# Kernel tuning notes

Measured on AMD Instinct MI355X. Metric: run time of the kernel, lower is better.

Reference implementation:

```python
import jax, jax.numpy as jnp
import numpy as np

HARD_NUM = 700      # hardcoded self.hard_num in HardOIMLoss
OIM_SCALAR = 30.0   # oim_scalar init arg
N, D, P, Q = 4096, 256, 5532, 5000


def _l2norm(x):
    return x / jnp.linalg.norm(x, axis=-1, keepdims=True)


def setup_inputs() -> dict:
    key = jax.random.key(0)
    k1, k2, k3, k4, k5 = jax.random.split(key, 5)
    # OIM features and lookup tables are L2-normalized rows
    inputs = _l2norm(jax.random.normal(k1, (N, D), dtype=jnp.float32))
    lut = _l2norm(jax.random.normal(k2, (P, D), dtype=jnp.float32))
    cq = _l2norm(jax.random.normal(k3, (Q, D), dtype=jnp.float32))
    reliability = jax.random.uniform(k4, (P + Q,), dtype=jnp.float32)
    labels = jax.random.randint(k5, (N,), 0, P, dtype=jnp.int32)
    return {"inputs": inputs, "labels": labels, "lut": lut, "cq": cq,
            "reliability": reliability}


def reference(inputs, labels, lut, cq, reliability):
    # projected[n, c] = <inputs_n, table_c> * reliability_c ;  table = [lut; cq]
    table = jnp.concatenate([lut, cq], axis=0)            # [P+Q, D]
    projected = (inputs @ table.T) * reliability[None, :]  # [N, P+Q]
    C = projected.shape[1]
    # value at sorted-descending index HARD_NUM == (HARD_NUM+1)-th largest
    boundary = jax.lax.top_k(projected, HARD_NUM + 1)[0][:, -1]  # [N]
    hard_mask = projected >= boundary[:, None]
    label_mask = jnp.arange(C, dtype=labels.dtype)[None, :] == labels[:, None]
    mask = hard_mask | label_mask
    logits = jnp.where(mask, projected * OIM_SCALAR, -jnp.inf)
    # cross entropy (mean over rows); label column is always unmasked
    logZ = jax.scipy.special.logsumexp(logits, axis=1)
    tgt = jnp.take_along_axis(logits, labels[:, None].astype(jnp.int32), axis=1)[:, 0]
    return jnp.mean(logZ - tgt)
```

## Files before the change

### kernel.cpp

```cpp
#include <hip/hip_runtime.h>
#include <math.h>

#define N_ROWS 4096
#define DIM    256
#define P_SZ   5532
#define Q_SZ   5000
#define C_COLS 10532
#define TPAD   10624
#define PSTR   10560
#define K_SEL  701
#define SCALAR 30.0f

typedef __attribute__((ext_vector_type(8))) short   short8;
typedef __attribute__((ext_vector_type(4))) float   float4_t;
typedef __attribute__((ext_vector_type(4))) unsigned short ushort4_t;
typedef __attribute__((ext_vector_type(8))) unsigned short ushort8_t;

__device__ __forceinline__ unsigned short f2bf(float f) {
    unsigned u = __float_as_uint(f);
    unsigned r = u + 0x7FFFu + ((u >> 16) & 1u);
    return (unsigned short)(r >> 16);
}
__device__ __forceinline__ float bf2f(unsigned short u) {
    return __uint_as_float((unsigned)u << 16);
}
__device__ __forceinline__ unsigned key16(unsigned short u) {
    return (u & 0x8000u) ? (unsigned)(~u & 0xFFFFu) : (unsigned)(u | 0x8000u);
}
__device__ __forceinline__ float key2f16(unsigned key) {
    unsigned short b = (key & 0x8000u) ? (unsigned short)(key & 0x7FFFu)
                                       : (unsigned short)(~key & 0xFFFFu);
    return bf2f(b);
}
__device__ __forceinline__ void gload16(const void* g, void* l) {
    __builtin_amdgcn_global_load_lds(
        (const __attribute__((address_space(1))) unsigned int*)g,
        (__attribute__((address_space(3))) unsigned int*)l, 16, 0, 0);
}

__device__ __forceinline__ unsigned suffix_above(unsigned s, int lane, int wid,
                                                 unsigned* wsum) {
    unsigned incl = s;
    #pragma unroll
    for (int off = 1; off < 64; off <<= 1) {
        unsigned v = __shfl_down(incl, off, 64);
        if (lane + off < 64) incl += v;
    }
    unsigned wtot = __shfl(incl, 0, 64);
    if (lane == 0) wsum[wid] = wtot;
    __syncthreads();
    unsigned tail = 0;
    for (int w = wid + 1; w < 4; ++w) tail += wsum[w];
    return tail + (incl - s);
}

#define NIN_G  (N_ROWS * DIM / 4)
#define NTAB_G (TPAD * DIM / 4)

__global__ __launch_bounds__(256) void convert_bf16(
    const float* __restrict__ inputs, const float* __restrict__ lut,
    const float* __restrict__ cq, unsigned short* __restrict__ in_bf,
    unsigned short* __restrict__ tab_bf)
{
    const int g = blockIdx.x * 256 + threadIdx.x;
    if (g >= NIN_G + NTAB_G) return;
    float4_t v;
    unsigned short* dst;
    if (g < NIN_G) {
        v = *(const float4_t*)&inputs[(size_t)g * 4];
        dst = in_bf + (size_t)g * 4;
    } else {
        const int t = g - NIN_G;
        const int row = t >> 6;
        const int c4  = (t & 63) * 4;
        if (row < P_SZ)        v = *(const float4_t*)&lut[(size_t)row * DIM + c4];
        else if (row < C_COLS) v = *(const float4_t*)&cq[(size_t)(row - P_SZ) * DIM + c4];
        else                   v = (float4_t){0.f, 0.f, 0.f, 0.f};
        dst = tab_bf + (size_t)t * 4;
    }
    ushort4_t h = { f2bf(v.x), f2bf(v.y), f2bf(v.z), f2bf(v.w) };
    *(ushort4_t*)dst = h;
}

#define NWG_X 83
#define NWG_Y 32
#define NWG   (NWG_X * NWG_Y)

__global__ __launch_bounds__(256) void gemm_proj(
    const unsigned short* __restrict__ in_bf,
    const unsigned short* __restrict__ tab_bf,
    const float* __restrict__ rel,
    unsigned short* __restrict__ proj)
{
    __shared__ __align__(16) unsigned short At[128 * 64];
    __shared__ __align__(16) unsigned short Bt[128 * 64];

    const int tid  = threadIdx.x;
    const int lane = tid & 63, wid = tid >> 6;
    const int wm = wid >> 1, wn = wid & 1;

    const int phys = blockIdx.x;
    const int wg   = (phys & 7) * (NWG / 8) + (phys >> 3);
    const int bx   = wg >> 5;
    const int by   = wg & 31;
    const int row0 = by * 128, col0 = bx * 128;

    float4_t acc[4][4];
    #pragma unroll
    for (int i = 0; i < 4; ++i)
        #pragma unroll
        for (int j = 0; j < 4; ++j)
            acc[i][j] = (float4_t){0.f, 0.f, 0.f, 0.f};

    for (int k0 = 0; k0 < DIM; k0 += 64) {
        #pragma unroll
        for (int it = 0; it < 4; ++it) {
            const int g  = it * 256 + tid;
            const int r  = g >> 3;
            const int kb = ((g & 7) * 16) ^ ((r & 7) << 4);
            gload16(in_bf  + (size_t)(row0 + r) * DIM + k0 + (kb >> 1),
                    (char*)At + g * 16);
            gload16(tab_bf + (size_t)(col0 + r) * DIM + k0 + (kb >> 1),
                    (char*)Bt + g * 16);
        }
        __syncthreads();

        #pragma unroll
        for (int kk = 0; kk < 2; ++kk) {
            const int krow = lane & 15;
            const int kb   = kk * 64 + ((lane >> 4) << 4);
            short8 af[4], bfr[4];
            #pragma unroll
            for (int i = 0; i < 4; ++i) {
                const int r = wm * 64 + i * 16 + krow;
                af[i] = *(const short8*)((const char*)At + (r * 128 + (kb ^ ((r & 7) << 4))));
            }
            #pragma unroll
            for (int j = 0; j < 4; ++j) {
                const int r = wn * 64 + j * 16 + krow;
                bfr[j] = *(const short8*)((const char*)Bt + (r * 128 + (kb ^ ((r & 7) << 4))));
            }
            #pragma unroll
            for (int i = 0; i < 4; ++i)
                #pragma unroll
                for (int j = 0; j < 4; ++j)
                    acc[i][j] = __builtin_amdgcn_mfma_f32_16x16x32_bf16(af[i], bfr[j], acc[i][j], 0, 0, 0);
        }
        __syncthreads();
    }

    const int lr = (lane >> 4) << 2;
    const int lc = lane & 15;
    #pragma unroll
    for (int j = 0; j < 4; ++j) {
        const int col = col0 + wn * 64 + j * 16 + lc;
        if (col >= PSTR) continue;
        const bool pad = (col >= C_COLS);
        const float rl = pad ? 0.f : rel[col];
        #pragma unroll
        for (int i = 0; i < 4; ++i) {
            const int row = row0 + wm * 64 + i * 16 + lr;
            #pragma unroll
            for (int rr = 0; rr < 4; ++rr)
                proj[(size_t)(row + rr) * PSTR + col] =
                    pad ? (unsigned short)0xFF80u
                        : f2bf(acc[i][j][rr] * rl);
        }
    }
}

__global__ __launch_bounds__(256) void row_loss_kernel(
    const unsigned short* __restrict__ proj, const int* __restrict__ labels,
    float* __restrict__ row_loss)
{
    __shared__ __align__(16) unsigned short vals[PSTR];
    __shared__ unsigned hist[2048];
    __shared__ unsigned wsum[4];
    __shared__ unsigned wred[4];
    __shared__ float fred[4];
    __shared__ unsigned sel_b, sel_k;

    const int tid = threadIdx.x, lane = tid & 63, wid = tid >> 6;
    const int row = blockIdx.x;
    const ushort8_t* prow = (const ushort8_t*)(proj + (size_t)row * PSTR);

    for (int i = tid; i < 2048; i += 256) hist[i] = 0;
    __syncthreads();

    unsigned mkey = 0;
    for (int g = tid; g < PSTR / 8; g += 256) {
        const ushort8_t v = prow[g];
        *(ushort8_t*)&vals[g * 8] = v;
        #pragma unroll
        for (int e = 0; e < 8; ++e) {
            const unsigned key = key16(v[e]);
            mkey = max(mkey, key);
            atomicAdd(&hist[key >> 5], 1u);
        }
    }
    #pragma unroll
    for (int off = 1; off < 64; off <<= 1) {
        const unsigned t = __shfl_down(mkey, off, 64);
        if (lane + off < 64) mkey = max(mkey, t);
    }
    if (lane == 0) wred[wid] = mkey;
    __syncthreads();
    mkey = max(max(wred[0], wred[1]), max(wred[2], wred[3]));
    const float m = key2f16(mkey);

    unsigned k = K_SEL;

    {
        unsigned s = 0;
        #pragma unroll
        for (int b = 0; b < 8; ++b) s += hist[tid * 8 + b];
        unsigned cum = suffix_above(s, lane, wid, wsum);
        #pragma unroll
        for (int b = 7; b >= 0; --b) {
            const unsigned c = hist[tid * 8 + b];
            if (cum < k && cum + c >= k) { sel_b = (unsigned)(tid * 8 + b); sel_k = k - cum; }
            cum += c;
        }
    }
    __syncthreads();
    const unsigned b1 = sel_b; k = sel_k;
    if (tid < 32) hist[tid] = 0;
    __syncthreads();

    for (int g = tid; g < PSTR / 8; g += 256) {
        const ushort8_t v = *(const ushort8_t*)&vals[g * 8];
        #pragma unroll
        for (int e = 0; e < 8; ++e) {
            const unsigned key = key16(v[e]);
            if ((key >> 5) == b1) atomicAdd(&hist[key & 31u], 1u);
        }
    }
    __syncthreads();
    if (wid == 0) {
        const unsigned c = (lane < 32) ? hist[lane] : 0u;
        unsigned incl = c;
        #pragma unroll
        for (int off = 1; off < 64; off <<= 1) {
            const unsigned t = __shfl_down(incl, off, 64);
            if (lane + off < 64) incl += t;
        }
        const unsigned above = incl - c;
        if (lane < 32 && above < k && above + c >= k) sel_b = (unsigned)lane;
    }
    __syncthreads();
    const unsigned bkey = (b1 << 5) | sel_b;

    const float c2 = SCALAR * 1.4426950408889634f;
    float s = 0.f;
    for (int g = tid; g < PSTR / 8; g += 256) {
        const ushort8_t v = *(const ushort8_t*)&vals[g * 8];
        #pragma unroll
        for (int e = 0; e < 8; ++e)
            if (key16(v[e]) >= bkey) s += exp2f(c2 * (bf2f(v[e]) - m));
    }
    #pragma unroll
    for (int off = 1; off < 64; off <<= 1) {
        const float t = __shfl_down(s, off, 64);
        if (lane + off < 64) s += t;
    }
    if (lane == 0) fred[wid] = s;
    __syncthreads();

    if (tid == 0) {
        float total = fred[0] + fred[1] + fred[2] + fred[3];
        const unsigned short ul = vals[labels[row]];
        const float pl = bf2f(ul);
        if (key16(ul) < bkey) total += exp2f(c2 * (pl - m));
        row_loss[row] = SCALAR * m + logf(total) - SCALAR * pl;
    }
}

__global__ __launch_bounds__(256) void final_reduce(
    const float* __restrict__ row_loss, float* __restrict__ out)
{
    __shared__ float fred[4];
    const int tid = threadIdx.x, lane = tid & 63, wid = tid >> 6;
    float s = 0.f;
    for (int i = tid; i < N_ROWS; i += 256) s += row_loss[i];
    #pragma unroll
    for (int off = 1; off < 64; off <<= 1) {
        const float t = __shfl_down(s, off, 64);
        if (lane + off < 64) s += t;
    }
    if (lane == 0) fred[wid] = s;
    __syncthreads();
    if (tid == 0) out[0] = (fred[0] + fred[1] + fred[2] + fred[3]) / (float)N_ROWS;
}

extern "C" void kernel_launch(void* const* d_in, const int* in_sizes, int n_in,
                              void* d_out, int out_size, void* d_ws, size_t ws_size,
                              hipStream_t stream) {
    const float* inputs = (const float*)d_in[0];
    const int*   labels = (const int*)d_in[1];
    const float* lut    = (const float*)d_in[2];
    const float* cq     = (const float*)d_in[3];
    const float* rel    = (const float*)d_in[4];
    float* out = (float*)d_out;

    unsigned short* in_bf  = (unsigned short*)d_ws;
    unsigned short* tab_bf = in_bf  + (size_t)N_ROWS * DIM;
    unsigned short* proj   = tab_bf + (size_t)TPAD * DIM;
    float* rl_buf = (float*)(proj + (size_t)N_ROWS * PSTR);

    convert_bf16<<<(NIN_G + NTAB_G) / 256, 256, 0, stream>>>(inputs, lut, cq, in_bf, tab_bf);
    gemm_proj<<<NWG, 256, 0, stream>>>(in_bf, tab_bf, rel, proj);
    row_loss_kernel<<<N_ROWS, 256, 0, stream>>>(proj, labels, rl_buf);
    final_reduce<<<1, 256, 0, stream>>>(rl_buf, out);
}
```

Measured before the change: 115.4 us.

## Fuse exp-sum into histogram pass with fixed max shift; stage GEMM output through LDS

The GEMM epilogue now writes its bf16 tile to LDS and stores it to global memory as coalesced 16-byte rows, with the projection stride padded to the table pad width. The row-loss kernel drops the max reduction and the LDS row copy. It accumulates per-bucket exp sums alongside the histogram counts, using a fixed shift of 1.0 (which relies on |projected| <= 1 for normalized inputs and reliability <= 1), so the separate final exp pass is removed. The cost is a float atomic plus an exp for every element in the first pass, and the second pass now rereads the row from global memory.

```diff
diff --git a/kernel.cpp b/kernel.cpp
--- a/kernel.cpp
+++ b/kernel.cpp
@@ -7,9 +7,11 @@
 #define Q_SZ   5000
 #define C_COLS 10532
 #define TPAD   10624
-#define PSTR   10560
+#define PSTR   10624
+#define NGR    (PSTR / 8)
 #define K_SEL  701
 #define SCALAR 30.0f
+#define C2     (SCALAR * 1.4426950408889634f)
 
 typedef __attribute__((ext_vector_type(8))) short   short8;
 typedef __attribute__((ext_vector_type(4))) float   float4_t;
@@ -27,31 +29,10 @@
 __device__ __forceinline__ unsigned key16(unsigned short u) {
     return (u & 0x8000u) ? (unsigned)(~u & 0xFFFFu) : (unsigned)(u | 0x8000u);
 }
-__device__ __forceinline__ float key2f16(unsigned key) {
-    unsigned short b = (key & 0x8000u) ? (unsigned short)(key & 0x7FFFu)
-                                       : (unsigned short)(~key & 0xFFFFu);
-    return bf2f(b);
-}
 __device__ __forceinline__ void gload16(const void* g, void* l) {
     __builtin_amdgcn_global_load_lds(
         (const __attribute__((address_space(1))) unsigned int*)g,
         (__attribute__((address_space(3))) unsigned int*)l, 16, 0, 0);
-}
-
-__device__ __forceinline__ unsigned suffix_above(unsigned s, int lane, int wid,
-                                                 unsigned* wsum) {
-    unsigned incl = s;
-    #pragma unroll
-    for (int off = 1; off < 64; off <<= 1) {
-        unsigned v = __shfl_down(incl, off, 64);
-        if (lane + off < 64) incl += v;
-    }
-    unsigned wtot = __shfl(incl, 0, 64);
-    if (lane == 0) wsum[wid] = wtot;
-    __syncthreads();
-    unsigned tail = 0;
-    for (int w = wid + 1; w < 4; ++w) tail += wsum[w];
-    return tail + (incl - s);
 }
 
 #define NIN_G  (N_ROWS * DIM / 4)
@@ -85,6 +66,7 @@
 #define NWG_X 83
 #define NWG_Y 32
 #define NWG   (NWG_X * NWG_Y)
+#define CSTR  132
 
 __global__ __launch_bounds__(256) void gemm_proj(
     const unsigned short* __restrict__ in_bf,
@@ -92,8 +74,9 @@
     const float* __restrict__ rel,
     unsigned short* __restrict__ proj)
 {
-    __shared__ __align__(16) unsigned short At[128 * 64];
-    __shared__ __align__(16) unsigned short Bt[128 * 64];
+    __shared__ __align__(16) unsigned short smem[128 * CSTR];
+    unsigned short* At = smem;
+    unsigned short* Bt = smem + 128 * 64;
 
     const int tid  = threadIdx.x;
     const int lane = tid & 63, wid = tid >> 6;
@@ -153,19 +136,27 @@
     const int lc = lane & 15;
     #pragma unroll
     for (int j = 0; j < 4; ++j) {
-        const int col = col0 + wn * 64 + j * 16 + lc;
-        if (col >= PSTR) continue;
+        const int cl  = wn * 64 + j * 16 + lc;
+        const int col = col0 + cl;
         const bool pad = (col >= C_COLS);
         const float rl = pad ? 0.f : rel[col];
         #pragma unroll
         for (int i = 0; i < 4; ++i) {
-            const int row = row0 + wm * 64 + i * 16 + lr;
+            const int rbase = wm * 64 + i * 16 + lr;
             #pragma unroll
             for (int rr = 0; rr < 4; ++rr)
-                proj[(size_t)(row + rr) * PSTR + col] =
-                    pad ? (unsigned short)0xFF80u
-                        : f2bf(acc[i][j][rr] * rl);
-        }
+                smem[(rbase + rr) * CSTR + cl] =
+                    pad ? (unsigned short)0xFF80u : f2bf(acc[i][j][rr] * rl);
+        }
+    }
+    __syncthreads();
+    #pragma unroll
+    for (int it = 0; it < 8; ++it) {
+        const int g = it * 256 + tid;
+        const int r = g >> 4;
+        const int c8 = (g & 15) * 8;
+        *(ushort8_t*)(proj + (size_t)(row0 + r) * PSTR + col0 + c8) =
+            *(const ushort8_t*)&smem[r * CSTR + c8];
     }
 }
 
@@ -173,105 +164,103 @@
     const unsigned short* __restrict__ proj, const int* __restrict__ labels,
     float* __restrict__ row_loss)
 {
-    __shared__ __align__(16) unsigned short vals[PSTR];
     __shared__ unsigned hist[2048];
+    __shared__ float    bexp[2048];
+    __shared__ unsigned h2[32];
+    __shared__ float    e2[32];
     __shared__ unsigned wsum[4];
-    __shared__ unsigned wred[4];
-    __shared__ float fred[4];
+    __shared__ float    fsum[4];
     __shared__ unsigned sel_b, sel_k;
+    __shared__ float    sel_major, sel_minor;
 
     const int tid = threadIdx.x, lane = tid & 63, wid = tid >> 6;
     const int row = blockIdx.x;
     const ushort8_t* prow = (const ushort8_t*)(proj + (size_t)row * PSTR);
 
-    for (int i = tid; i < 2048; i += 256) hist[i] = 0;
-    __syncthreads();
-
-    unsigned mkey = 0;
-    for (int g = tid; g < PSTR / 8; g += 256) {
+    #pragma unroll
+    for (int i = tid; i < 2048; i += 256) { hist[i] = 0; bexp[i] = 0.f; }
+    if (tid < 32) { h2[tid] = 0; e2[tid] = 0.f; }
+    __syncthreads();
+
+    for (int g = tid; g < NGR; g += 256) {
         const ushort8_t v = prow[g];
-        *(ushort8_t*)&vals[g * 8] = v;
         #pragma unroll
         for (int e = 0; e < 8; ++e) {
             const unsigned key = key16(v[e]);
-            mkey = max(mkey, key);
+            const float ex = exp2f(C2 * (bf2f(v[e]) - 1.0f));
             atomicAdd(&hist[key >> 5], 1u);
-        }
-    }
-    #pragma unroll
-    for (int off = 1; off < 64; off <<= 1) {
-        const unsigned t = __shfl_down(mkey, off, 64);
-        if (lane + off < 64) mkey = max(mkey, t);
-    }
-    if (lane == 0) wred[wid] = mkey;
-    __syncthreads();
-    mkey = max(max(wred[0], wred[1]), max(wred[2], wred[3]));
-    const float m = key2f16(mkey);
-
-    unsigned k = K_SEL;
+            atomicAdd(&bexp[key >> 5], ex);
+        }
+    }
+    __syncthreads();
 
     {
-        unsigned s = 0;
-        #pragma unroll
-        for (int b = 0; b < 8; ++b) s += hist[tid * 8 + b];
-        unsigned cum = suffix_above(s, lane, wid, wsum);
+        const int t8 = tid * 8;
+        unsigned s = 0; float f = 0.f;
+        #pragma unroll
+        for (int b = 0; b < 8; ++b) { s += hist[t8 + b]; f += bexp[t8 + b]; }
+        unsigned ic = s; float fc = f;
+        #pragma unroll
+        for (int off = 1; off < 64; off <<= 1) {
+            const unsigned tc = __shfl_down(ic, off, 64);
+            const float    tf = __shfl_down(fc, off, 64);
+            if (lane + off < 64) { ic += tc; fc += tf; }
+        }
+        if (lane == 0) { wsum[wid] = ic; fsum[wid] = fc; }
+        __syncthreads();
+        unsigned cum = ic - s; float fcum = fc - f;
+        for (int w = wid + 1; w < 4; ++w) { cum += wsum[w]; fcum += fsum[w]; }
         #pragma unroll
         for (int b = 7; b >= 0; --b) {
-            const unsigned c = hist[tid * 8 + b];
-            if (cum < k && cum + c >= k) { sel_b = (unsigned)(tid * 8 + b); sel_k = k - cum; }
-            cum += c;
-        }
-    }
-    __syncthreads();
-    const unsigned b1 = sel_b; k = sel_k;
-    if (tid < 32) hist[tid] = 0;
-    __syncthreads();
-
-    for (int g = tid; g < PSTR / 8; g += 256) {
-        const ushort8_t v = *(const ushort8_t*)&vals[g * 8];
+            const unsigned c = hist[t8 + b];
+            if (cum < K_SEL && cum + c >= K_SEL) {
+                sel_b = (unsigned)(t8 + b); sel_k = K_SEL - cum; sel_major = fcum;
+            }
+            cum += c; fcum += bexp[t8 + b];
+        }
+    }
+    __syncthreads();
+    const unsigned b1 = sel_b;
+    const unsigned k2 = sel_k;
+    __syncthreads();
+
+    for (int g = tid; g < NGR; g += 256) {
+        const ushort8_t v = prow[g];
         #pragma unroll
         for (int e = 0; e < 8; ++e) {
             const unsigned key = key16(v[e]);
-            if ((key >> 5) == b1) atomicAdd(&hist[key & 31u], 1u);
+            if ((key >> 5) == b1) {
+                atomicAdd(&h2[key & 31u], 1u);
+                atomicAdd(&e2[key & 31u], exp2f(C2 * (bf2f(v[e]) - 1.0f)));
+            }
         }
     }
     __syncthreads();
     if (wid == 0) {
-        const unsigned c = (lane < 32) ? hist[lane] : 0u;
-        unsigned incl = c;
+        const unsigned c = (lane < 32) ? h2[lane] : 0u;
+        const float    f = (lane < 32) ? e2[lane] : 0.f;
+        unsigned ic = c; float fc = f;
         #pragma unroll
         for (int off = 1; off < 64; off <<= 1) {
-            const unsigned t = __shfl_down(incl, off, 64);
-            if (lane + off < 64) incl += t;
-        }
-        const unsigned above = incl - c;
-        if (lane < 32 && above < k && above + c >= k) sel_b = (unsigned)lane;
-    }
-    __syncthreads();
-    const unsigned bkey = (b1 << 5) | sel_b;
-
-    const float c2 = SCALAR * 1.4426950408889634f;
-    float s = 0.f;
-    for (int g = tid; g < PSTR / 8; g += 256) {
-        const ushort8_t v = *(const ushort8_t*)&vals[g * 8];
-        #pragma unroll
-        for (int e = 0; e < 8; ++e)
-            if (key16(v[e]) >= bkey) s += exp2f(c2 * (bf2f(v[e]) - m));
-    }
-    #pragma unroll
-    for (int off = 1; off < 64; off <<= 1) {
-        const float t = __shfl_down(s, off, 64);
-        if (lane + off < 64) s += t;
-    }
-    if (lane == 0) fred[wid] = s;
+            const unsigned tc = __shfl_down(ic, off, 64);
+            const float    tf = __shfl_down(fc, off, 64);
+            if (lane + off < 64) { ic += tc; fc += tf; }
+        }
+        const unsigned above = ic - c;
+        if (lane < 32 && above < k2 && above + c >= k2) {
+            sel_b = (unsigned)lane; sel_minor = fc;
+        }
+    }
     __syncthreads();
 
     if (tid == 0) {
-        float total = fred[0] + fred[1] + fred[2] + fred[3];
-        const unsigned short ul = vals[labels[row]];
+        const unsigned bkey = (b1 << 5) | sel_b;
+        float total = sel_major + sel_minor;
+        const unsigned short ul = *(const unsigned short*)
+            ((const unsigned short*)prow + labels[row]);
         const float pl = bf2f(ul);
-        if (key16(ul) < bkey) total += exp2f(c2 * (pl - m));
-        row_loss[row] = SCALAR * m + logf(total) - SCALAR * pl;
+        if (key16(ul) < bkey) total += exp2f(C2 * (pl - 1.0f));
+        row_loss[row] = SCALAR * 1.0f + logf(total) - SCALAR * pl;
     }
 }
 
```

New measurement: 310.6 us. 169% more time.
